# Performance work log

Hardware: AMD Instinct MI355X
Metric: run time of the kernel (lower is better)

The kernel has to match this reference:

```python
import jax, jax.numpy as jnp
import numpy as np

DIM = 96       # d_model / channels
DSTATE = 16    # SSM state size N
DINNER = 2 * DIM   # expand=2 -> 192
DTRANK = 6     # ceil(DIM/16)
K = 4          # scan directions
B, H, W = 2, 56, 56


def _ln(x, g, b, eps=1e-5):
    m = x.mean(-1, keepdims=True)
    v = x.var(-1, keepdims=True)
    return (x - m) * jax.lax.rsqrt(v + eps) * g + b


def _dwconv3(x, w, b):  # x [B,C,H,W], w [C,1,3,3] depthwise, SAME padding
    y = jax.lax.conv_general_dilated(x, w, (1, 1), [(1, 1), (1, 1)],
                                     feature_group_count=x.shape[1],
                                     dimension_numbers=('NCHW', 'OIHW', 'NCHW'))
    return y + b[None, :, None, None]


def _bn(x, g, b, m, v, eps=1e-5):  # eval-mode BatchNorm2d on NCHW
    inv = jax.lax.rsqrt(v + eps)
    return (x - m[None, :, None, None]) * (inv * g)[None, :, None, None] + b[None, :, None, None]


def _selective_scan(u, dt, A, Bs, Cs, Dp, dt_bias):
    # u, dt: [B,K,D,L]; A: [K,D,N]; Bs,Cs: [B,K,N,L]; Dp, dt_bias: [K,D]
    dt = jax.nn.softplus(dt + dt_bias[None, :, :, None])
    dA = jnp.exp(jnp.einsum('bkdl,kdn->lbkdn', dt, A))           # [L,B,K,D,N]
    dBu = jnp.einsum('bkdl,bknl,bkdl->lbkdn', dt, Bs, u)          # [L,B,K,D,N]
    Ct = jnp.moveaxis(Cs, -1, 0)                                  # [L,B,K,N]
    h0 = jnp.zeros(dA.shape[1:], dA.dtype)

    def step(h, inp):
        dA_l, dBu_l, C_l = inp
        h = dA_l * h + dBu_l
        return h, jnp.einsum('bkdn,bkn->bkd', h, C_l)

    _, ys = jax.lax.scan(step, h0, (dA, dBu, Ct))                 # ys [L,B,K,D]
    return jnp.moveaxis(ys, 0, -1) + u * Dp[None, :, :, None]     # [B,K,D,L]


def setup_inputs() -> dict:
    key = jax.random.key(0)
    ks = jax.random.split(key, 12)
    s = 0.02
    f32 = jnp.float32
    inp = {}
    inp['x'] = jax.random.normal(ks[0], (B, H, W, DIM), f32)
    # conv branch: depthwise 3x3 + BN + ReLU + 1x1 + BN
    inp['dw_w'] = jax.random.normal(ks[1], (DIM, 1, 3, 3), f32) * s
    inp['dw_b'] = jnp.zeros((DIM,), f32)
    inp['bn1_g'] = jnp.ones((DIM,), f32); inp['bn1_b'] = jnp.zeros((DIM,), f32)
    inp['bn1_m'] = jnp.zeros((DIM,), f32); inp['bn1_v'] = jnp.ones((DIM,), f32)
    inp['pw_w'] = jax.random.normal(ks[2], (DIM, DIM), f32) * s
    inp['pw_b'] = jnp.zeros((DIM,), f32)
    inp['bn2_g'] = jnp.ones((DIM,), f32); inp['bn2_b'] = jnp.zeros((DIM,), f32)
    inp['bn2_m'] = jnp.zeros((DIM,), f32); inp['bn2_v'] = jnp.ones((DIM,), f32)
    # pre-mamba LayerNorm
    inp['ln_g'] = jnp.ones((DIM,), f32); inp['ln_b'] = jnp.zeros((DIM,), f32)
    # SS2D params
    inp['in_proj_w'] = jax.random.normal(ks[3], (2 * DINNER, DIM), f32) * s
    inp['conv_w'] = jax.random.normal(ks[4], (DINNER, 1, 3, 3), f32) * s
    inp['conv_b'] = jnp.zeros((DINNER,), f32)
    inp['x_proj_w'] = jax.random.normal(ks[5], (K, DTRANK + 2 * DSTATE, DINNER), f32) * s
    inp['dt_w'] = jax.random.normal(ks[6], (K, DINNER, DTRANK), f32) * s
    inp['dt_b'] = jnp.full((K, DINNER), -4.6, f32)  # softplus(dt_b) ~= 0.01
    inp['A_logs'] = jnp.log(jnp.tile(jnp.arange(1, DSTATE + 1, dtype=f32), (K * DINNER, 1)))
    inp['Ds'] = jnp.ones((K * DINNER,), f32)
    inp['out_norm_g'] = jnp.ones((DINNER,), f32); inp['out_norm_b'] = jnp.zeros((DINNER,), f32)
    inp['out_proj_w'] = jax.random.normal(ks[7], (DIM, DINNER), f32) * s
    # fusion: Linear(2*dim, dim) + LayerNorm(dim)
    inp['fus_w'] = jax.random.normal(ks[8], (DIM, 2 * DIM), f32) * s
    inp['fus_b'] = jnp.zeros((DIM,), f32)
    inp['fus_ln_g'] = jnp.ones((DIM,), f32); inp['fus_ln_b'] = jnp.zeros((DIM,), f32)
    return inp


def reference(x, dw_w, dw_b, bn1_g, bn1_b, bn1_m, bn1_v, pw_w, pw_b,
              bn2_g, bn2_b, bn2_m, bn2_v, ln_g, ln_b,
              in_proj_w, conv_w, conv_b, x_proj_w, dt_w, dt_b, A_logs, Ds,
              out_norm_g, out_norm_b, out_proj_w, fus_w, fus_b, fus_ln_g, fus_ln_b):
    Bsz, Hh, Ww, C = x.shape
    L = Hh * Ww
    # ----- conv branch -----
    xc = jnp.transpose(x, (0, 3, 1, 2))                       # [B,C,H,W]
    c = jax.nn.relu(_bn(_dwconv3(xc, dw_w, dw_b), bn1_g, bn1_b, bn1_m, bn1_v))
    c = jnp.einsum('bchw,oc->bohw', c, pw_w) + pw_b[None, :, None, None]
    conv_out = jnp.transpose(_bn(c, bn2_g, bn2_b, bn2_m, bn2_v), (0, 2, 3, 1))
    # ----- mamba (SS2D) branch -----
    xn = _ln(x, ln_g, ln_b)
    xz = xn @ in_proj_w.T                                     # [B,H,W,2*Din]
    xm, z = jnp.split(xz, 2, axis=-1)
    xm = jnp.transpose(xm, (0, 3, 1, 2))                      # [B,Din,H,W]
    xm = jax.nn.silu(_dwconv3(xm, conv_w, conv_b))
    v1 = xm.reshape(Bsz, DINNER, L)                           # row-major scan
    v2 = jnp.transpose(xm, (0, 1, 3, 2)).reshape(Bsz, DINNER, L)  # col-major scan
    xs = jnp.stack([v1, v2, v1[..., ::-1], v2[..., ::-1]], axis=1)  # [B,4,Din,L]
    x_dbl = jnp.einsum('bkdl,kcd->bkcl', xs, x_proj_w)
    dts, Bmat, Cmat = jnp.split(x_dbl, [DTRANK, DTRANK + DSTATE], axis=2)
    dts = jnp.einsum('bkrl,kdr->bkdl', dts, dt_w)
    A = -jnp.exp(A_logs).reshape(K, DINNER, DSTATE)
    out_y = _selective_scan(xs, dts, A, Bmat, Cmat, Ds.reshape(K, DINNER), dt_b)
    y1 = out_y[:, 0]
    inv_y = out_y[:, 2:4][..., ::-1]
    y2 = inv_y[:, 0]
    y3 = jnp.transpose(inv_y[:, 1].reshape(Bsz, DINNER, Ww, Hh), (0, 1, 3, 2)).reshape(Bsz, DINNER, L)
    y4 = jnp.transpose(out_y[:, 1].reshape(Bsz, DINNER, Ww, Hh), (0, 1, 3, 2)).reshape(Bsz, DINNER, L)
    y = jnp.transpose(y1 + y2 + y3 + y4, (0, 2, 1)).reshape(Bsz, Hh, Ww, DINNER)
    y = _ln(y, out_norm_g, out_norm_b)
    y = y * jax.nn.silu(z)
    mamba_out = y @ out_proj_w.T                              # [B,H,W,C]
    # ----- fusion + residual -----
    fused = jnp.concatenate([conv_out, mamba_out], axis=-1) @ fus_w.T + fus_b
    fused = _ln(fused, fus_ln_g, fus_ln_b)
    return x + fused
```

## Files before the change

kernel.cpp:

```cpp
#include <hip/hip_runtime.h>
#include <math.h>

#define BZ 2
#define HH 56
#define WW 56
#define LL 3136
#define CC 96
#define DI 192
#define NS 16
#define RR 6
#define NT 49
#define NCH 98
#define CH 32

#define OFF_CONV   0
#define OFF_XMRAW  602112
#define OFF_Z      1806336
#define OFF_V1     3010560
#define OFF_V2     4214784
#define OFF_DT     5419008
#define OFF_BS     10235904
#define OFF_CS     10637312
#define OFF_Y      11038720
#define OFF_Y13    15855616
#define OFF_T      18264064
#define OFF_W2     19468288

__device__ __forceinline__ float softplusf(float x) {
    if (x > 20.f) return x;
    return log1pf(__expf(x));
}

__global__ __launch_bounds__(64) void k0_w2(const float* __restrict__ fus_w,
                                            const float* __restrict__ opw,
                                            float* __restrict__ W2) {
    int i = blockIdx.x * 64 + threadIdx.x;
    if (i >= CC * DI) return;
    int o = i / DI, d = i % DI;
    float acc = 0.f;
    for (int j = 0; j < CC; ++j)
        acc += fus_w[o * DI + CC + j] * opw[j * DI + d];
    W2[i] = acc;
}

__global__ __launch_bounds__(256) void k0c_negA(const float* __restrict__ A_logs,
                                                float* __restrict__ negA) {
    int i = blockIdx.x * 256 + threadIdx.x;
    if (i < 4 * DI * NS) negA[i] = -__expf(A_logs[i]);
}

__global__ __launch_bounds__(256) void k1a_dw(const float* __restrict__ x,
    const float* __restrict__ dw_w, const float* __restrict__ dw_b,
    const float* __restrict__ bn1_g, const float* __restrict__ bn1_b,
    const float* __restrict__ bn1_m, const float* __restrict__ bn1_v,
    float* __restrict__ cbuf) {
    int i = blockIdx.x * 256 + threadIdx.x;
    if (i >= BZ * LL * CC) return;
    int c = i % CC;
    int bl = i / CC;
    int l = bl % LL, b = bl / LL;
    int h = l / WW, w = l % WW;
    float acc = dw_b[c];
    #pragma unroll
    for (int dy = -1; dy <= 1; ++dy) {
        int hh = h + dy; if (hh < 0 || hh >= HH) continue;
        #pragma unroll
        for (int dx = -1; dx <= 1; ++dx) {
            int ww = w + dx; if (ww < 0 || ww >= WW) continue;
            acc += x[((b * HH + hh) * WW + ww) * CC + c] * dw_w[c * 9 + (dy + 1) * 3 + (dx + 1)];
        }
    }
    float inv = rsqrtf(bn1_v[c] + 1e-5f);
    float v = (acc - bn1_m[c]) * inv * bn1_g[c] + bn1_b[c];
    cbuf[i] = fmaxf(v, 0.f);
}

__global__ __launch_bounds__(256) void k1b_pw(const float* __restrict__ cbuf,
    const float* __restrict__ pw_w, const float* __restrict__ pw_b,
    const float* __restrict__ bn2_g, const float* __restrict__ bn2_b,
    const float* __restrict__ bn2_m, const float* __restrict__ bn2_v,
    float* __restrict__ conv_out) {
    int t0 = blockIdx.x * 64;
    int b = blockIdx.y;
    int lane = threadIdx.x & 63;
    int wvu = __builtin_amdgcn_readfirstlane(threadIdx.x >> 6);
    __shared__ float ct[CC * 65];
    __shared__ float res[64 * 97];
    const float* cb = cbuf + (b * LL + t0) * CC;
    for (int e = threadIdx.x; e < 64 * CC; e += 256) {
        int p = e / CC, c = e % CC;
        ct[c * 65 + p] = cb[e];
    }
    __syncthreads();
    float acc[24];
    const float* pb = pw_b + wvu * 24;
    #pragma unroll
    for (int j = 0; j < 24; ++j) acc[j] = pb[j];
    const float* wb = pw_w + (wvu * 24) * CC;
    for (int c = 0; c < CC; ++c) {
        float xv = ct[c * 65 + lane];
        #pragma unroll
        for (int j = 0; j < 24; ++j)
            acc[j] += xv * wb[j * CC + c];
    }
    #pragma unroll
    for (int j = 0; j < 24; ++j) {
        int o = wvu * 24 + j;
        float inv = rsqrtf(bn2_v[o] + 1e-5f);
        res[lane * 97 + o] = (acc[j] - bn2_m[o]) * inv * bn2_g[o] + bn2_b[o];
    }
    __syncthreads();
    float* ob = conv_out + (b * LL + t0) * CC;
    for (int e = threadIdx.x; e < 64 * CC; e += 256) {
        int pl = e / CC, o = e % CC;
        ob[e] = res[pl * 97 + o];
    }
}

__global__ __launch_bounds__(256) void k2_inproj(const float* __restrict__ x,
    const float* __restrict__ ln_g, const float* __restrict__ ln_b,
    const float* __restrict__ ipw,
    float* __restrict__ xm_raw, float* __restrict__ z_buf) {
    int t0 = blockIdx.x * 64;
    int og = blockIdx.y;
    int b = blockIdx.z;
    int lane = threadIdx.x & 63;
    int wv = threadIdx.x >> 6;
    int wvu = __builtin_amdgcn_readfirstlane(wv);
    __shared__ float xt[64 * 97];
    __shared__ float xn[96 * 65];
    __shared__ float ps[4][64], ps2[4][64];
    const float* xb = x + (b * LL + t0) * CC;
    for (int e = threadIdx.x; e < 64 * CC; e += 256) {
        int p = e / CC, c = e % CC;
        xt[p * 97 + c] = xb[e];
    }
    __syncthreads();
    float s = 0.f, s2 = 0.f;
    #pragma unroll
    for (int j = 0; j < 24; ++j) {
        float v = xt[lane * 97 + wvu * 24 + j];
        s += v; s2 += v * v;
    }
    ps[wv][lane] = s; ps2[wv][lane] = s2;
    __syncthreads();
    float st = 0.f, st2 = 0.f;
    #pragma unroll
    for (int i = 0; i < 4; ++i) { st += ps[i][lane]; st2 += ps2[i][lane]; }
    float m = st * (1.f / 96.f);
    float inv = rsqrtf(st2 * (1.f / 96.f) - m * m + 1e-5f);
    #pragma unroll
    for (int j = 0; j < 24; ++j) {
        int c = wvu * 24 + j;
        xn[c * 65 + lane] = (xt[lane * 97 + c] - m) * inv * ln_g[c] + ln_b[c];
    }
    __syncthreads();
    float acc[12];
    #pragma unroll
    for (int j = 0; j < 12; ++j) acc[j] = 0.f;
    int o0 = og * 48 + wvu * 12;
    const float* wbase = ipw + o0 * CC;
    for (int c = 0; c < CC; ++c) {
        float xv = xn[c * 65 + lane];
        #pragma unroll
        for (int j = 0; j < 12; ++j)
            acc[j] += xv * wbase[j * CC + c];
    }
    int p = t0 + lane;
    #pragma unroll
    for (int j = 0; j < 12; ++j) {
        int out = o0 + j;
        if (out < DI) xm_raw[(b * DI + out) * LL + p] = acc[j];
        else          z_buf[(b * DI + (out - DI)) * LL + p] = acc[j];
    }
}

__global__ __launch_bounds__(256) void k3_dw(const float* __restrict__ xm_raw,
    const float* __restrict__ conv_w, const float* __restrict__ conv_b,
    float* __restrict__ v1, float* __restrict__ v2) {
    int bd = blockIdx.x;
    int half = blockIdx.y;
    int d = bd % DI;
    int h0 = half * 28;
    __shared__ float tile[28 * 57];
    const float* src = xm_raw + bd * LL;
    float wloc[9];
    #pragma unroll
    for (int i = 0; i < 9; ++i) wloc[i] = conv_w[d * 9 + i];
    float bias = conv_b[d];
    for (int e = threadIdx.x; e < 28 * WW; e += 256) {
        int hl = e / WW, w = e % WW;
        int h = h0 + hl;
        float acc = bias;
        #pragma unroll
        for (int dy = -1; dy <= 1; ++dy) {
            int hh = h + dy; if (hh < 0 || hh >= HH) continue;
            #pragma unroll
            for (int dx = -1; dx <= 1; ++dx) {
                int ww = w + dx; if (ww < 0 || ww >= WW) continue;
                acc += src[hh * WW + ww] * wloc[(dy + 1) * 3 + (dx + 1)];
            }
        }
        float sig = 1.f / (1.f + __expf(-acc));
        float v = acc * sig;
        v1[bd * LL + h * WW + w] = v;
        tile[hl * 57 + w] = v;
    }
    __syncthreads();
    for (int e = threadIdx.x; e < 28 * WW; e += 256) {
        int w = e / 28, hl = e % 28;
        v2[bd * LL + w * HH + h0 + hl] = tile[hl * 57 + w];
    }
}

__global__ __launch_bounds__(256) void k4_proj(const float* __restrict__ v1,
    const float* __restrict__ v2, const float* __restrict__ xpw,
    const float* __restrict__ dtw, const float* __restrict__ dtb,
    float* __restrict__ dt_s, float* __restrict__ B_s, float* __restrict__ C_s) {
    int t0 = blockIdx.x * 64;
    int ky = blockIdx.y;
    int k = ky >> 1, half = ky & 1;
    int b = blockIdx.z;
    int lane = threadIdx.x & 63;
    int wvu = __builtin_amdgcn_readfirstlane(threadIdx.x >> 6);
    __shared__ float xs_l[DI * 64];
    __shared__ float dtr[RR * 64];
    const float* src = ((k & 1) == 0 ? v1 : v2) + b * DI * LL + t0;
    for (int e = threadIdx.x; e < DI * 64; e += 256) {
        int d = e >> 6, p = e & 63;
        xs_l[e] = src[d * LL + p];
    }
    __syncthreads();
    int rl = wvu * 5; if (rl > 14) rl = 14;
    int r0 = half * 19 + rl;
    float acc[5];
    #pragma unroll
    for (int i = 0; i < 5; ++i) acc[i] = 0.f;
    const float* wbase = xpw + (k * 38 + r0) * DI;
    for (int d = 0; d < DI; ++d) {
        float xv = xs_l[d * 64 + lane];
        #pragma unroll
        for (int i = 0; i < 5; ++i)
            acc[i] += xv * wbase[i * DI + d];
    }
    int p = t0 + lane;
    #pragma unroll
    for (int i = 0; i < 5; ++i) {
        int c = r0 + i;
        if (c < RR) {
            dtr[c * 64 + lane] = acc[i];
        } else if (c < RR + NS) {
            B_s[((b * 4 + k) * NS + (c - RR)) * LL + p] = acc[i];
        } else {
            C_s[((b * 4 + k) * NS + (c - RR - NS)) * LL + p] = acc[i];
        }
    }
    __syncthreads();
    if (half == 0) {
        for (int i = 0; i < 48; ++i) {
            int d = wvu * 48 + i;
            float a = dtb[k * DI + d];
            const float* wr = dtw + (k * DI + d) * RR;
            #pragma unroll
            for (int r = 0; r < RR; ++r)
                a += dtr[r * 64 + lane] * wr[r];
            dt_s[((b * 4 + k) * DI + d) * LL + p] = softplusf(a);
        }
    }
}

template<bool FWD>
__global__ __launch_bounds__(64, 2) void k5a_scan(const float* __restrict__ dt_s,
    const float* __restrict__ B_s, const float* __restrict__ C_s,
    const float* __restrict__ v1, const float* __restrict__ v2,
    const float* __restrict__ A_logs, float* __restrict__ y_scan,
    float* __restrict__ hl_buf, float* __restrict__ Tbuf, int kbase) {
    int bx = blockIdx.x;
    int dg = bx % 3, c = bx / 3;
    int k = kbase + blockIdx.y;
    int b = blockIdx.z;
    int bk = b * 4 + k;
    int lane = threadIdx.x;
    int d0 = dg * 64, d = d0 + lane;
    int s0 = FWD ? c * CH : (LL - (c + 1) * CH);
    __shared__ float bc[CH * 36];
    float Ae[16];
    const float* ap = A_logs + (k * DI + d) * NS;
    #pragma unroll
    for (int n = 0; n < 16; ++n) Ae[n] = -__expf(ap[n]) * 1.442695040888963f;
    const float4* dtp4 = (const float4*)(dt_s + (bk * DI + d) * LL + s0);
    const float4* up4  = (const float4*)((((k & 1) == 0) ? v1 : v2) + (b * DI + d) * LL + s0);
    float4 dt4[8], u4[8];
    #pragma unroll
    for (int i = 0; i < 8; ++i) { dt4[i] = dtp4[i]; u4[i] = up4[i]; }
    float* dts = (float*)dt4;
    float* us  = (float*)u4;
    int pr = lane >> 5, pc = lane & 31;
    #pragma unroll
    for (int i = 0; i < 8; ++i) {
        int nn = i * 2 + pr;
        bc[pc * 36 + nn]      = B_s[(bk * NS + nn) * LL + s0 + pc];
        bc[pc * 36 + 16 + nn] = C_s[(bk * NS + nn) * LL + s0 + pc];
    }
    __syncthreads();
    float h[16];
    #pragma unroll
    for (int n = 0; n < 16; ++n) h[n] = 0.f;
    float cum = 0.f;
    #pragma unroll
    for (int jj = 0; jj < CH; ++jj) {
        const int j = FWD ? jj : CH - 1 - jj;
        float dtv = dts[j];
        float uv  = us[j];
        float du = dtv * uv;
        cum += dtv;
        const float4* row4 = (const float4*)&bc[j * 36];
        float4 b0 = row4[0], b1 = row4[1], b2 = row4[2], b3 = row4[3];
        float4 c0 = row4[4], c1 = row4[5], c2 = row4[6], c3 = row4[7];
        float bv[16] = {b0.x,b0.y,b0.z,b0.w, b1.x,b1.y,b1.z,b1.w,
                        b2.x,b2.y,b2.z,b2.w, b3.x,b3.y,b3.z,b3.w};
        float cv[16] = {c0.x,c0.y,c0.z,c0.w, c1.x,c1.y,c1.z,c1.w,
                        c2.x,c2.y,c2.z,c2.w, c3.x,c3.y,c3.z,c3.w};
        float y = 0.f;
        #pragma unroll
        for (int n = 0; n < 16; ++n) {
            h[n] = exp2f(dtv * Ae[n]) * h[n] + du * bv[n];
            y += h[n] * cv[n];
        }
        us[j] = y;
    }
    float4* yp4 = (float4*)(y_scan + (bk * DI + d) * LL + s0);
    #pragma unroll
    for (int i = 0; i < 8; ++i) yp4[i] = u4[i];
    float4* hp4 = (float4*)(hl_buf + (bk * NCH + c) * (DI * NS) + d * NS);
    hp4[0] = make_float4(h[0], h[1], h[2], h[3]);
    hp4[1] = make_float4(h[4], h[5], h[6], h[7]);
    hp4[2] = make_float4(h[8], h[9], h[10], h[11]);
    hp4[3] = make_float4(h[12], h[13], h[14], h[15]);
    Tbuf[(bk * NCH + c) * DI + d] = cum;
}

__global__ __launch_bounds__(64) void k5c_comb(float* __restrict__ hl_buf,
    const float* __restrict__ Tbuf, const float* __restrict__ negA) {
    int dg = blockIdx.x, k = blockIdx.y, b = blockIdx.z;
    int lane = threadIdx.x, dl = lane >> 4, n = lane & 15;
    int d = dg * 4 + dl;
    int bk = b * 4 + k;
    float Av = negA[(k * DI + d) * NS + n];
    float H = 0.f;
    float* slot0 = hl_buf + (bk * NCH + 0) * (DI * NS) + dg * 64 + lane;
    float hl_next = *slot0;
    float T_next = Tbuf[(bk * NCH + 0) * DI + d];
    for (int c = 0; c < NCH; ++c) {
        float hl = hl_next, T = T_next;
        if (c + 1 < NCH) {
            hl_next = hl_buf[(bk * NCH + c + 1) * (DI * NS) + dg * 64 + lane];
            T_next  = Tbuf[(bk * NCH + c + 1) * DI + d];
        }
        hl_buf[(bk * NCH + c) * (DI * NS) + dg * 64 + lane] = H;
        H = hl + __expf(Av * T) * H;
    }
}

__global__ __launch_bounds__(256) void k5d_corr(const float* __restrict__ dt_s,
    const float* __restrict__ C_s, const float* __restrict__ hin,
    const float* __restrict__ negA, float* __restrict__ y_scan) {
    int t = blockIdx.x;
    int k = blockIdx.y, b = blockIdx.z;
    bool fwd = (k < 2);
    int c  = fwd ? (t + 1) : (NCH - 1 - t);
    int s0 = fwd ? (t + 1) * CH : t * CH;
    int p32 = threadIdx.x & 31, sl = threadIdx.x >> 5;
    int bk = b * 4 + k;
    __shared__ float c_l[16 * 33];
    for (int e = threadIdx.x; e < 16 * CH; e += 256) {
        int n = e >> 5, s = e & 31;
        c_l[n * 33 + s] = C_s[(bk * NS + n) * LL + s0 + s];
    }
    __syncthreads();
    for (int j = 0; j < 24; ++j) {
        int d = sl * 24 + j;
        float dtv = dt_s[(bk * DI + d) * LL + s0 + p32];
        float cum = dtv;
        if (fwd) {
            #pragma unroll
            for (int off = 1; off < 32; off <<= 1) {
                float o = __shfl_up(cum, off, 32);
                if (p32 >= off) cum += o;
            }
        } else {
            #pragma unroll
            for (int off = 1; off < 32; off <<= 1) {
                float o = __shfl_down(cum, off, 32);
                if (p32 < 32 - off) cum += o;
            }
        }
        const float* hp = hin + (bk * NCH + c) * (DI * NS) + d * 16;
        const float* ap = negA + (k * DI + d) * NS;
        float acc = 0.f;
        #pragma unroll
        for (int n = 0; n < 16; ++n) {
            acc += c_l[n * 33 + p32] * __expf(ap[n] * cum) * hp[n];
        }
        y_scan[(bk * DI + d) * LL + s0 + p32] += acc;
    }
}

__global__ __launch_bounds__(256) void k5b_tr(const float* __restrict__ y_scan,
                                              float* __restrict__ y13t) {
    int idx = blockIdx.x;
    int d = idx % DI;
    int bk = idx / DI;
    int kk = bk % 2, b = bk / 2;
    int k = (kk == 0) ? 1 : 3;
    __shared__ float tile[HH * 57];
    const float* src = y_scan + ((b * 4 + k) * DI + d) * LL;
    for (int e = threadIdx.x; e < LL; e += 256) {
        int w = e / HH, h = e % HH;
        tile[h * 57 + w] = src[e];
    }
    __syncthreads();
    float* dst = y13t + idx * LL;
    for (int e = threadIdx.x; e < LL; e += 256) {
        int h = e / WW, w = e % WW;
        dst[e] = tile[h * 57 + w];
    }
}

__global__ __launch_bounds__(256) void k6_gather(const float* __restrict__ y_scan,
    const float* __restrict__ y13t, const float* __restrict__ v1,
    const float* __restrict__ z_buf, const float* __restrict__ Ds,
    const float* __restrict__ ong, const float* __restrict__ onb,
    float* __restrict__ t_buf) {
    int t0 = blockIdx.x * 16;
    int b = blockIdx.y;
    int p16 = threadIdx.x & 15, sl = threadIdx.x >> 4;
    int p = t0 + p16;
    __shared__ float yv[DI * 17];
    __shared__ float ps[16][16], ps2[16][16];
    float s = 0.f, s2 = 0.f;
    for (int j = 0; j < 12; ++j) {
        int d = sl * 12 + j;
        float dsum = Ds[d] + Ds[DI + d] + Ds[2 * DI + d] + Ds[3 * DI + d];
        float val = y_scan[((b * 4 + 0) * DI + d) * LL + p]
                  + y_scan[((b * 4 + 2) * DI + d) * LL + p]
                  + y13t[((b * 2 + 0) * DI + d) * LL + p]
                  + y13t[((b * 2 + 1) * DI + d) * LL + p]
                  + v1[(b * DI + d) * LL + p] * dsum;
        yv[d * 17 + p16] = val;
        s += val; s2 += val * val;
    }
    ps[sl][p16] = s; ps2[sl][p16] = s2;
    __syncthreads();
    float st = 0.f, st2 = 0.f;
    #pragma unroll
    for (int i = 0; i < 16; ++i) { st += ps[i][p16]; st2 += ps2[i][p16]; }
    float m = st * (1.f / 192.f);
    float inv = rsqrtf(st2 * (1.f / 192.f) - m * m + 1e-5f);
    for (int j = 0; j < 12; ++j) {
        int d = sl * 12 + j;
        float val = (yv[d * 17 + p16] - m) * inv * ong[d] + onb[d];
        float zz = z_buf[(b * DI + d) * LL + p];
        float sig = 1.f / (1.f + __expf(-zz));
        t_buf[(b * DI + d) * LL + p] = val * zz * sig;
    }
}

__global__ __launch_bounds__(256) void k7a_mm(const float* __restrict__ t_buf,
    const float* __restrict__ conv_out, const float* __restrict__ W2,
    const float* __restrict__ fus_w, const float* __restrict__ fus_b,
    float* __restrict__ fusedT) {
    int t0 = blockIdx.x * 64;
    int og = blockIdx.y;
    int b = blockIdx.z;
    int lane = threadIdx.x & 63;
    int wvu = __builtin_amdgcn_readfirstlane(threadIdx.x >> 6);
    __shared__ float ct[CC * 65];
    const float* cb = conv_out + (b * LL + t0) * CC;
    for (int e = threadIdx.x; e < 64 * CC; e += 256) {
        int p = e / CC, c = e % CC;
        ct[c * 65 + p] = cb[e];
    }
    __syncthreads();
    int o0 = og * 12 + wvu * 3;
    float acc[3];
    #pragma unroll
    for (int j = 0; j < 3; ++j) acc[j] = fus_b[o0 + j];
    int p = t0 + lane;
    const float* w2 = W2 + o0 * DI;
    for (int d = 0; d < DI; ++d) {
        float tv = t_buf[(b * DI + d) * LL + p];
        #pragma unroll
        for (int j = 0; j < 3; ++j)
            acc[j] += tv * w2[j * DI + d];
    }
    const float* fw = fus_w + o0 * DI;
    for (int c = 0; c < CC; ++c) {
        float cv = ct[c * 65 + lane];
        #pragma unroll
        for (int j = 0; j < 3; ++j)
            acc[j] += cv * fw[j * DI + c];
    }
    #pragma unroll
    for (int j = 0; j < 3; ++j)
        fusedT[(b * CC + o0 + j) * LL + p] = acc[j];
}

__global__ __launch_bounds__(256) void k7b_ln(const float* __restrict__ fusedT,
    const float* __restrict__ flg, const float* __restrict__ flb,
    const float* __restrict__ x, float* __restrict__ out) {
    int t0 = blockIdx.x * 16;
    int b = blockIdx.y;
    int p16 = threadIdx.x & 15, sl = threadIdx.x >> 4;
    __shared__ float ft[CC * 17];
    __shared__ float res[16 * 97];
    __shared__ float ps[16][16], ps2[16][16];
    for (int e = threadIdx.x; e < CC * 16; e += 256) {
        int o = e >> 4, p = e & 15;
        ft[o * 17 + p] = fusedT[(b * CC + o) * LL + t0 + p];
    }
    __syncthreads();
    float s = 0.f, s2 = 0.f;
    #pragma unroll
    for (int j = 0; j < 6; ++j) {
        float v = ft[(sl * 6 + j) * 17 + p16];
        s += v; s2 += v * v;
    }
    ps[sl][p16] = s; ps2[sl][p16] = s2;
    __syncthreads();
    float st = 0.f, st2 = 0.f;
    #pragma unroll
    for (int i = 0; i < 16; ++i) { st += ps[i][p16]; st2 += ps2[i][p16]; }
    float m = st * (1.f / 96.f);
    float inv = rsqrtf(st2 * (1.f / 96.f) - m * m + 1e-5f);
    #pragma unroll
    for (int j = 0; j < 6; ++j) {
        int o = sl * 6 + j;
        res[p16 * 97 + o] = (ft[o * 17 + p16] - m) * inv * flg[o] + flb[o];
    }
    __syncthreads();
    const float* xb = x + (b * LL + t0) * CC;
    float* ob = out + (b * LL + t0) * CC;
    for (int e = threadIdx.x; e < 16 * CC; e += 256) {
        int pl = e / CC, o = e % CC;
        ob[e] = xb[e] + res[pl * 97 + o];
    }
}

extern "C" void kernel_launch(void* const* d_in, const int* in_sizes, int n_in,
                              void* d_out, int out_size, void* d_ws, size_t ws_size,
                              hipStream_t stream) {
    const float* x        = (const float*)d_in[0];
    const float* dw_w     = (const float*)d_in[1];
    const float* dw_b     = (const float*)d_in[2];
    const float* bn1_g    = (const float*)d_in[3];
    const float* bn1_b    = (const float*)d_in[4];
    const float* bn1_m    = (const float*)d_in[5];
    const float* bn1_v    = (const float*)d_in[6];
    const float* pw_w     = (const float*)d_in[7];
    const float* pw_b     = (const float*)d_in[8];
    const float* bn2_g    = (const float*)d_in[9];
    const float* bn2_b    = (const float*)d_in[10];
    const float* bn2_m    = (const float*)d_in[11];
    const float* bn2_v    = (const float*)d_in[12];
    const float* ln_g     = (const float*)d_in[13];
    const float* ln_b     = (const float*)d_in[14];
    const float* ipw      = (const float*)d_in[15];
    const float* conv_w   = (const float*)d_in[16];
    const float* conv_b   = (const float*)d_in[17];
    const float* xpw      = (const float*)d_in[18];
    const float* dtw      = (const float*)d_in[19];
    const float* dtb      = (const float*)d_in[20];
    const float* A_logs   = (const float*)d_in[21];
    const float* Ds       = (const float*)d_in[22];
    const float* ong      = (const float*)d_in[23];
    const float* onb      = (const float*)d_in[24];
    const float* opw      = (const float*)d_in[25];
    const float* fus_w    = (const float*)d_in[26];
    const float* fus_b    = (const float*)d_in[27];
    const float* flg      = (const float*)d_in[28];
    const float* flb      = (const float*)d_in[29];

    float* ws = (float*)d_ws;
    float* conv_out = ws + OFF_CONV;
    float* xm_raw   = ws + OFF_XMRAW;
    float* z_buf    = ws + OFF_Z;
    float* v1       = ws + OFF_V1;
    float* v2       = ws + OFF_V2;
    float* dt_s     = ws + OFF_DT;
    float* B_s      = ws + OFF_BS;
    float* C_s      = ws + OFF_CS;
    float* y_scan   = ws + OFF_Y;
    float* y13t     = ws + OFF_Y13;
    float* t_buf    = ws + OFF_T;
    float* W2       = ws + OFF_W2;
    float* cbuf     = y13t;
    float* hl_buf   = y13t;
    float* Tbuf     = xm_raw;
    float* negA     = B_s;
    float* fusedT   = y13t;
    float* out      = (float*)d_out;

    k0_w2<<<dim3((CC * DI + 63) / 64), dim3(64), 0, stream>>>(fus_w, opw, W2);
    k1a_dw<<<dim3((BZ * LL * CC + 255) / 256), dim3(256), 0, stream>>>(x, dw_w, dw_b,
                                                     bn1_g, bn1_b, bn1_m, bn1_v, cbuf);
    k1b_pw<<<dim3(NT, BZ), dim3(256), 0, stream>>>(cbuf, pw_w, pw_b,
                                                   bn2_g, bn2_b, bn2_m, bn2_v, conv_out);
    k2_inproj<<<dim3(NT, 8, BZ), dim3(256), 0, stream>>>(x, ln_g, ln_b, ipw, xm_raw, z_buf);
    k3_dw<<<dim3(BZ * DI, 2), dim3(256), 0, stream>>>(xm_raw, conv_w, conv_b, v1, v2);
    k4_proj<<<dim3(NT, 8, BZ), dim3(256), 0, stream>>>(v1, v2, xpw, dtw, dtb, dt_s, B_s, C_s);
    k5a_scan<true><<<dim3(3 * NCH, 2, BZ), dim3(64), 0, stream>>>(dt_s, B_s, C_s, v1, v2, A_logs,
                                                            y_scan, hl_buf, Tbuf, 0);
    k5a_scan<false><<<dim3(3 * NCH, 2, BZ), dim3(64), 0, stream>>>(dt_s, B_s, C_s, v1, v2, A_logs,
                                                            y_scan, hl_buf, Tbuf, 2);
    k0c_negA<<<dim3(48), dim3(256), 0, stream>>>(A_logs, negA);
    k5c_comb<<<dim3(48, 4, BZ), dim3(64), 0, stream>>>(hl_buf, Tbuf, negA);
    k5d_corr<<<dim3(NCH - 1, 4, BZ), dim3(256), 0, stream>>>(dt_s, C_s, hl_buf, negA, y_scan);
    k5b_tr<<<dim3(BZ * 2 * DI), dim3(256), 0, stream>>>(y_scan, y13t);
    k6_gather<<<dim3(196, BZ), dim3(256), 0, stream>>>(y_scan, y13t, v1, z_buf, Ds, ong, onb, t_buf);
    k7a_mm<<<dim3(NT, 8, BZ), dim3(256), 0, stream>>>(t_buf, conv_out, W2, fus_w, fus_b, fusedT);
    k7b_ln<<<dim3(196, BZ), dim3(256), 0, stream>>>(fusedT, flg, flb, x, out);
}
```

Baseline: 379.1 us.

## Split projection kernels and merge scan directions into one launch for more parallelism

The pointwise conv kernel now splits its output channels across two blocks, so the grid doubles and each thread holds fewer accumulators. The x_proj kernel is split in two. The first part is a 64-thread kernel that reads activations straight from global memory and writes the dt-rank intermediates to a workspace buffer. The second part is a separate dt kernel that applies dt_w and softplus. The forward and backward scan launches are merged into one launch that picks its direction at runtime, using a macro-unrolled step. The aim is more blocks in flight and fewer launches, at the cost of an extra global round trip for the dt-rank values and redundant global reads in the xproj kernel.

```diff
diff --git a/kernel.cpp b/kernel.cpp
--- a/kernel.cpp
+++ b/kernel.cpp
@@ -81,39 +81,41 @@
     const float* __restrict__ bn2_m, const float* __restrict__ bn2_v,
     float* __restrict__ conv_out) {
     int t0 = blockIdx.x * 64;
-    int b = blockIdx.y;
+    int og = blockIdx.y;
+    int b = blockIdx.z;
     int lane = threadIdx.x & 63;
     int wvu = __builtin_amdgcn_readfirstlane(threadIdx.x >> 6);
     __shared__ float ct[CC * 65];
-    __shared__ float res[64 * 97];
+    __shared__ float res[64 * 49];
     const float* cb = cbuf + (b * LL + t0) * CC;
     for (int e = threadIdx.x; e < 64 * CC; e += 256) {
         int p = e / CC, c = e % CC;
         ct[c * 65 + p] = cb[e];
     }
     __syncthreads();
-    float acc[24];
-    const float* pb = pw_b + wvu * 24;
-    #pragma unroll
-    for (int j = 0; j < 24; ++j) acc[j] = pb[j];
-    const float* wb = pw_w + (wvu * 24) * CC;
+    int o0 = og * 48 + wvu * 12;
+    float acc[12];
+    const float* pb = pw_b + o0;
+    #pragma unroll
+    for (int j = 0; j < 12; ++j) acc[j] = pb[j];
+    const float* wb = pw_w + o0 * CC;
     for (int c = 0; c < CC; ++c) {
         float xv = ct[c * 65 + lane];
         #pragma unroll
-        for (int j = 0; j < 24; ++j)
+        for (int j = 0; j < 12; ++j)
             acc[j] += xv * wb[j * CC + c];
     }
     #pragma unroll
-    for (int j = 0; j < 24; ++j) {
-        int o = wvu * 24 + j;
+    for (int j = 0; j < 12; ++j) {
+        int o = o0 + j;
         float inv = rsqrtf(bn2_v[o] + 1e-5f);
-        res[lane * 97 + o] = (acc[j] - bn2_m[o]) * inv * bn2_g[o] + bn2_b[o];
-    }
-    __syncthreads();
-    float* ob = conv_out + (b * LL + t0) * CC;
-    for (int e = threadIdx.x; e < 64 * CC; e += 256) {
-        int pl = e / CC, o = e % CC;
-        ob[e] = res[pl * 97 + o];
+        res[lane * 49 + wvu * 12 + j] = (acc[j] - bn2_m[o]) * inv * bn2_g[o] + bn2_b[o];
+    }
+    __syncthreads();
+    float* ob = conv_out + (b * LL + t0) * CC + og * 48;
+    for (int e = threadIdx.x; e < 64 * 48; e += 256) {
+        int pl = e / 48, o = e % 48;
+        ob[pl * CC + o] = res[pl * 49 + o];
     }
 }
 
@@ -213,76 +215,98 @@
     }
 }
 
-__global__ __launch_bounds__(256) void k4_proj(const float* __restrict__ v1,
+__global__ __launch_bounds__(64) void k4a_xproj(const float* __restrict__ v1,
     const float* __restrict__ v2, const float* __restrict__ xpw,
-    const float* __restrict__ dtw, const float* __restrict__ dtb,
-    float* __restrict__ dt_s, float* __restrict__ B_s, float* __restrict__ C_s) {
-    int t0 = blockIdx.x * 64;
-    int ky = blockIdx.y;
-    int k = ky >> 1, half = ky & 1;
-    int b = blockIdx.z;
-    int lane = threadIdx.x & 63;
-    int wvu = __builtin_amdgcn_readfirstlane(threadIdx.x >> 6);
-    __shared__ float xs_l[DI * 64];
-    __shared__ float dtr[RR * 64];
+    float* __restrict__ dtr_g, float* __restrict__ B_s, float* __restrict__ C_s) {
+    int bx = blockIdx.x;
+    int tile = bx >> 3, rg = bx & 7;
+    int k = blockIdx.y, b = blockIdx.z;
+    int lane = threadIdx.x;
+    int t0 = tile * 64;
+    int r0 = rg * 5; if (r0 > 33) r0 = 33;
     const float* src = ((k & 1) == 0 ? v1 : v2) + b * DI * LL + t0;
-    for (int e = threadIdx.x; e < DI * 64; e += 256) {
-        int d = e >> 6, p = e & 63;
-        xs_l[e] = src[d * LL + p];
-    }
-    __syncthreads();
-    int rl = wvu * 5; if (rl > 14) rl = 14;
-    int r0 = half * 19 + rl;
     float acc[5];
     #pragma unroll
     for (int i = 0; i < 5; ++i) acc[i] = 0.f;
     const float* wbase = xpw + (k * 38 + r0) * DI;
     for (int d = 0; d < DI; ++d) {
-        float xv = xs_l[d * 64 + lane];
+        float xv = src[d * LL + lane];
         #pragma unroll
         for (int i = 0; i < 5; ++i)
             acc[i] += xv * wbase[i * DI + d];
     }
+    int bk = b * 4 + k;
     int p = t0 + lane;
     #pragma unroll
     for (int i = 0; i < 5; ++i) {
         int c = r0 + i;
         if (c < RR) {
-            dtr[c * 64 + lane] = acc[i];
+            dtr_g[(bk * RR + c) * LL + p] = acc[i];
         } else if (c < RR + NS) {
-            B_s[((b * 4 + k) * NS + (c - RR)) * LL + p] = acc[i];
+            B_s[(bk * NS + (c - RR)) * LL + p] = acc[i];
         } else {
-            C_s[((b * 4 + k) * NS + (c - RR - NS)) * LL + p] = acc[i];
+            C_s[(bk * NS + (c - RR - NS)) * LL + p] = acc[i];
         }
     }
-    __syncthreads();
-    if (half == 0) {
-        for (int i = 0; i < 48; ++i) {
-            int d = wvu * 48 + i;
-            float a = dtb[k * DI + d];
-            const float* wr = dtw + (k * DI + d) * RR;
-            #pragma unroll
-            for (int r = 0; r < RR; ++r)
-                a += dtr[r * 64 + lane] * wr[r];
-            dt_s[((b * 4 + k) * DI + d) * LL + p] = softplusf(a);
-        }
-    }
-}
-
-template<bool FWD>
+}
+
+__global__ __launch_bounds__(256) void k4b_dt(const float* __restrict__ dtr_g,
+    const float* __restrict__ dtw, const float* __restrict__ dtb,
+    float* __restrict__ dt_s) {
+    int t0 = blockIdx.x * 64;
+    int k = blockIdx.y, b = blockIdx.z;
+    int lane = threadIdx.x & 63;
+    int wvu = __builtin_amdgcn_readfirstlane(threadIdx.x >> 6);
+    int bk = b * 4 + k;
+    int p = t0 + lane;
+    float r[RR];
+    #pragma unroll
+    for (int i = 0; i < RR; ++i) r[i] = dtr_g[(bk * RR + i) * LL + p];
+    for (int i = 0; i < 48; ++i) {
+        int d = wvu * 48 + i;
+        float a = dtb[k * DI + d];
+        const float* wr = dtw + (k * DI + d) * RR;
+        #pragma unroll
+        for (int q = 0; q < RR; ++q)
+            a += r[q] * wr[q];
+        dt_s[(bk * DI + d) * LL + p] = softplusf(a);
+    }
+}
+
+#define K5A_STEP(J) { \
+    float dtv = dts[J]; \
+    float uv  = us[J]; \
+    float du = dtv * uv; \
+    cum += dtv; \
+    const float4* row4 = (const float4*)&bc[(J) * 36]; \
+    float4 b0 = row4[0], b1 = row4[1], b2 = row4[2], b3 = row4[3]; \
+    float4 c0 = row4[4], c1 = row4[5], c2 = row4[6], c3 = row4[7]; \
+    float bv[16] = {b0.x,b0.y,b0.z,b0.w, b1.x,b1.y,b1.z,b1.w, \
+                    b2.x,b2.y,b2.z,b2.w, b3.x,b3.y,b3.z,b3.w}; \
+    float cv[16] = {c0.x,c0.y,c0.z,c0.w, c1.x,c1.y,c1.z,c1.w, \
+                    c2.x,c2.y,c2.z,c2.w, c3.x,c3.y,c3.z,c3.w}; \
+    float y = 0.f; \
+    _Pragma("unroll") \
+    for (int n = 0; n < 16; ++n) { \
+        h[n] = exp2f(dtv * Ae[n]) * h[n] + du * bv[n]; \
+        y += h[n] * cv[n]; \
+    } \
+    us[J] = y; }
+
 __global__ __launch_bounds__(64, 2) void k5a_scan(const float* __restrict__ dt_s,
     const float* __restrict__ B_s, const float* __restrict__ C_s,
     const float* __restrict__ v1, const float* __restrict__ v2,
     const float* __restrict__ A_logs, float* __restrict__ y_scan,
-    float* __restrict__ hl_buf, float* __restrict__ Tbuf, int kbase) {
+    float* __restrict__ hl_buf, float* __restrict__ Tbuf) {
     int bx = blockIdx.x;
     int dg = bx % 3, c = bx / 3;
-    int k = kbase + blockIdx.y;
+    int k = blockIdx.y;
     int b = blockIdx.z;
     int bk = b * 4 + k;
     int lane = threadIdx.x;
     int d0 = dg * 64, d = d0 + lane;
-    int s0 = FWD ? c * CH : (LL - (c + 1) * CH);
+    bool fwd = (k < 2);
+    int s0 = fwd ? c * CH : (LL - (c + 1) * CH);
     __shared__ float bc[CH * 36];
     float Ae[16];
     const float* ap = A_logs + (k * DI + d) * NS;
@@ -307,27 +331,12 @@
     #pragma unroll
     for (int n = 0; n < 16; ++n) h[n] = 0.f;
     float cum = 0.f;
-    #pragma unroll
-    for (int jj = 0; jj < CH; ++jj) {
-        const int j = FWD ? jj : CH - 1 - jj;
-        float dtv = dts[j];
-        float uv  = us[j];
-        float du = dtv * uv;
-        cum += dtv;
-        const float4* row4 = (const float4*)&bc[j * 36];
-        float4 b0 = row4[0], b1 = row4[1], b2 = row4[2], b3 = row4[3];
-        float4 c0 = row4[4], c1 = row4[5], c2 = row4[6], c3 = row4[7];
-        float bv[16] = {b0.x,b0.y,b0.z,b0.w, b1.x,b1.y,b1.z,b1.w,
-                        b2.x,b2.y,b2.z,b2.w, b3.x,b3.y,b3.z,b3.w};
-        float cv[16] = {c0.x,c0.y,c0.z,c0.w, c1.x,c1.y,c1.z,c1.w,
-                        c2.x,c2.y,c2.z,c2.w, c3.x,c3.y,c3.z,c3.w};
-        float y = 0.f;
-        #pragma unroll
-        for (int n = 0; n < 16; ++n) {
-            h[n] = exp2f(dtv * Ae[n]) * h[n] + du * bv[n];
-            y += h[n] * cv[n];
-        }
-        us[j] = y;
+    if (fwd) {
+        #pragma unroll
+        for (int j = 0; j < CH; ++j) K5A_STEP(j)
+    } else {
+        #pragma unroll
+        for (int jj = 0; jj < CH; ++jj) { const int j = CH - 1 - jj; K5A_STEP(j) }
     }
     float4* yp4 = (float4*)(y_scan + (bk * DI + d) * LL + s0);
     #pragma unroll
@@ -597,6 +606,7 @@
     float* cbuf     = y13t;
     float* hl_buf   = y13t;
     float* Tbuf     = xm_raw;
+    float* dtr_g    = xm_raw + 262144;
     float* negA     = B_s;
     float* fusedT   = y13t;
     float* out      = (float*)d_out;
@@ -604,15 +614,14 @@
     k0_w2<<<dim3((CC * DI + 63) / 64), dim3(64), 0, stream>>>(fus_w, opw, W2);
     k1a_dw<<<dim3((BZ * LL * CC + 255) / 256), dim3(256), 0, stream>>>(x, dw_w, dw_b,
                                                      bn1_g, bn1_b, bn1_m, bn1_v, cbuf);
-    k1b_pw<<<dim3(NT, BZ), dim3(256), 0, stream>>>(cbuf, pw_w, pw_b,
+    k1b_pw<<<dim3(NT, 2, BZ), dim3(256), 0, stream>>>(cbuf, pw_w, pw_b,
                                                    bn2_g, bn2_b, bn2_m, bn2_v, conv_out);
     k2_inproj<<<dim3(NT, 8, BZ), dim3(256), 0, stream>>>(x, ln_g, ln_b, ipw, xm_raw, z_buf);
     k3_dw<<<dim3(BZ * DI, 2), dim3(256), 0, stream>>>(xm_raw, conv_w, conv_b, v1, v2);
-    k4_proj<<<dim3(NT, 8, BZ), dim3(256), 0, stream>>>(v1, v2, xpw, dtw, dtb, dt_s, B_s, C_s);
-    k5a_scan<true><<<dim3(3 * NCH, 2, BZ), dim3(64), 0, stream>>>(dt_s, B_s, C_s, v1, v2, A_logs,
-                                                            y_scan, hl_buf, Tbuf, 0);
-    k5a_scan<false><<<dim3(3 * NCH, 2, BZ), dim3(64), 0, stream>>>(dt_s, B_s, C_s, v1, v2, A_logs,
-                                                            y_scan, hl_buf, Tbuf, 2);
+    k4a_xproj<<<dim3(NT * 8, 4, BZ), dim3(64), 0, stream>>>(v1, v2, xpw, dtr_g, B_s, C_s);
+    k4b_dt<<<dim3(NT, 4, BZ), dim3(256), 0, stream>>>(dtr_g, dtw, dtb, dt_s);
+    k5a_scan<<<dim3(3 * NCH, 4, BZ), dim3(64), 0, stream>>>(dt_s, B_s, C_s, v1, v2, A_logs,
+                                                            y_scan, hl_buf, Tbuf);
     k0c_negA<<<dim3(48), dim3(256), 0, stream>>>(A_logs, negA);
     k5c_comb<<<dim3(48, 4, BZ), dim3(64), 0, stream>>>(hl_buf, Tbuf, negA);
     k5d_corr<<<dim3(NCH - 1, 4, BZ), dim3(256), 0, stream>>>(dt_s, C_s, hl_buf, negA, y_scan);
```

New measurement: 419.5 us. +10.7%, slower.
